# Kernel optimization log

Hardware: AMD Instinct MI355X
Metric: run time of the kernel (lower is better)

## Reference

```python
import jax, jax.numpy as jnp
import numpy as np
import math

HEAD_DIM = 64
RP_DIM = 256
B, H, N = 4, 8, 4096
EPS = 1e-4  # performer positive-feature epsilon


def _ortho_gaussian_matrix(m, d, seed=0):
    # gaussian_orthogonal_random_matrix, scaling=0: stack QR-orthogonalized
    # d x d gaussian blocks, scale rows by norms of an iid gaussian matrix.
    rng = np.random.default_rng(seed)
    blocks = []
    for _ in range(int(np.ceil(m / d))):
        g = rng.standard_normal((d, d))
        q, _ = np.linalg.qr(g)
        blocks.append(q.T)
    mat = np.concatenate(blocks, axis=0)[:m]
    multiplier = np.linalg.norm(rng.standard_normal((m, d)), axis=1)
    return (multiplier[:, None] * mat).astype(np.float32)


def _softmax_features(x, proj, is_query):
    # FAVOR+ positive random features: ratio * exp(Wx - ||x||^2/2 - stab) + eps
    ratio = proj.shape[0] ** -0.5
    xp = jnp.einsum('bhnd,md->bhnm', x, proj)
    diag = 0.5 * jnp.sum(x * x, axis=-1, keepdims=True)
    if is_query:
        stab = jnp.max(xp, axis=-1, keepdims=True)
    else:
        stab = jnp.max(xp, axis=(-1, -2), keepdims=True)
    return ratio * (jnp.exp(xp - diag - stab) + EPS)


def setup_inputs() -> dict:
    key = jax.random.key(0)
    kq, kk, kv = jax.random.split(key, 3)
    Q = jax.random.normal(kq, (B, H, N, HEAD_DIM), dtype=jnp.float32)
    K = jax.random.normal(kk, (B, H, N, HEAD_DIM), dtype=jnp.float32)
    V = jax.random.normal(kv, (B, H, N, HEAD_DIM), dtype=jnp.float32)
    mask = jnp.ones((B, N), dtype=jnp.float32)
    projection = jnp.asarray(_ortho_gaussian_matrix(RP_DIM, HEAD_DIM, seed=0))
    return {'Q': Q, 'K': K, 'V': V, 'mask': mask, 'projection': projection}


def reference(Q, K, V, mask, projection):
    scale = HEAD_DIM ** -0.25  # 1/sqrt(sqrt(head_dim))
    m = mask[:, None, :, None]
    q = Q * scale
    k = K * scale * m
    v = V * m
    phi_q = _softmax_features(q, projection, is_query=True)   # [b,h,n,m]
    phi_k = _softmax_features(k, projection, is_query=False)  # [b,h,n,m]
    # non-causal linear attention
    k_sum = jnp.sum(phi_k, axis=2)                                   # [b,h,m]
    D_inv = 1.0 / jnp.einsum('bhnm,bhm->bhn', phi_q, k_sum)          # [b,h,n]
    context = jnp.einsum('bhnm,bhne->bhme', phi_k, v)                # [b,h,m,e]
    out = jnp.einsum('bhme,bhnm,bhn->bhne', context, phi_q, D_inv)   # [b,h,n,e]
    return out
```

## Files before the change

kernel.cpp:

```cpp
#include <hip/hip_runtime.h>
#include <hip/hip_bf16.h>


typedef __attribute__((ext_vector_type(8))) short short8;
typedef __attribute__((ext_vector_type(4))) float floatx4;

constexpr int BB = 4, HH = 8, NN = 4096, DD = 64, MM = 256, BH = 32;
constexpr float SCALE = 0.3535533905932738f;
constexpr float RATIO = 0.0625f;
constexpr float EPSI  = 1e-4f;
constexpr float NEGINF = -3.4e38f;

__device__ inline unsigned pk2(float a, float b) {
  unsigned ua = __float_as_uint(a) + 0x8000u;
  unsigned ub = __float_as_uint(b) + 0x8000u;
  return (ua >> 16) | (ub & 0xffff0000u);
}
__device__ inline float hif(float x) {
  return __uint_as_float((__float_as_uint(x) + 0x8000u) & 0xffff0000u);
}
__device__ inline unsigned short bhi(float x) {
  return (unsigned short)((__float_as_uint(x) + 0x8000u) >> 16);
}

union Frag { short8 s8; unsigned u[4]; };

__device__ inline void atomicMaxF(float* a, float v) {
  unsigned* ai = (unsigned*)a;
  unsigned old = __atomic_load_n(ai, __ATOMIC_RELAXED);
  while (__uint_as_float(old) < v) {
    unsigned assumed = old;
    old = atomicCAS(ai, assumed, __float_as_uint(v));
    if (old == assumed) break;
  }
}

__global__ __launch_bounds__(256) void prep_kernel(
    const float* __restrict__ proj, unsigned short* __restrict__ projH,
    unsigned short* __restrict__ projL, float* __restrict__ stabk) {
  const int i = blockIdx.x * 256 + threadIdx.x;
  float v = proj[i];
  projH[i] = bhi(v);
  projL[i] = bhi(v - hif(v));
  if (i < BH) stabk[i] = NEGINF;
}

__global__ __launch_bounds__(256) void vsum_kernel(
    const float* __restrict__ V, const float* __restrict__ mask,
    float* __restrict__ Vs) {
  const int bh = blockIdx.y, b = bh >> 3, t = threadIdx.x;
  const int e = t & 63, g = t >> 6;
  const int n0 = blockIdx.x * 128;
  float s = 0.f;
  for (int n = n0 + g; n < n0 + 128; n += 4)
    s += V[((size_t)bh * NN + n) * DD + e] * mask[b * NN + n];
  __shared__ float red[256];
  red[t] = s;
  __syncthreads();
  if (t < 64)
    atomicAdd(&Vs[bh * DD + t], (red[t] + red[t + 64]) + (red[t + 128] + red[t + 192]));
}

__global__ __launch_bounds__(256) void kside_kernel(
    const float* __restrict__ K, const float* __restrict__ V,
    const float* __restrict__ mask, const float* __restrict__ proj,
    float* __restrict__ stabk, float* __restrict__ ksE,
    float* __restrict__ ctxE) {
  const int bh = blockIdx.y, b = bh >> 3;
  const int t = threadIdx.x;
  const int w = t >> 6, l = t & 63, c = l & 15, sq = l >> 4;
  const int m0 = w * 64;

  __shared__ __align__(16) unsigned short sKs[2][32 * 72];
  __shared__ __align__(16) unsigned short sVt[2][64 * 40];
  __shared__ float sDiag[32];
  __shared__ float sRed[4];
  __shared__ __align__(16) unsigned short sPhi[4][4][2][512];

  Frag Bp[4][2][2];
#pragma unroll
  for (int tt = 0; tt < 4; ++tt)
#pragma unroll
    for (int s = 0; s < 2; ++s) {
      const float* pp = proj + (m0 + tt * 16 + c) * DD + s * 32 + sq * 8;
      float4 x0 = *(const float4*)pp;
      float4 x1 = *(const float4*)(pp + 4);
      float v[8] = {x0.x, x0.y, x0.z, x0.w, x1.x, x1.y, x1.z, x1.w};
#pragma unroll
      for (int j = 0; j < 4; ++j) {
        Bp[tt][s][0].u[j] = pk2(v[2 * j], v[2 * j + 1]);
        float l0 = v[2 * j] - hif(v[2 * j]);
        float l1 = v[2 * j + 1] - hif(v[2 * j + 1]);
        Bp[tt][s][1].u[j] = pk2(l0, l1);
      }
    }

  floatx4 ctxacc[4][4];
#pragma unroll
  for (int i = 0; i < 4; ++i)
#pragma unroll
    for (int j = 0; j < 4; ++j) ctxacc[i][j] = (floatx4){0.f, 0.f, 0.f, 0.f};
  float ksac[4] = {0.f, 0.f, 0.f, 0.f};
  float mxloc = NEGINF;

  const int r0 = blockIdx.x * 256;

  for (int ch = 0; ch < 8; ++ch) {
    const int rb = r0 + ch * 32;
    __syncthreads();

#pragma unroll
    for (int rep = 0; rep < 2; ++rep) {
      const int f = t + rep * 256;
      const int n = f >> 4, dg = f & 15;
      const float mk = mask[b * NN + rb + n];
      const float msc = mk * SCALE;
      float4 kv = *(const float4*)(K + ((size_t)bh * NN + rb + n) * DD + dg * 4);
      float k0 = kv.x * msc, k1 = kv.y * msc, k2 = kv.z * msc, k3 = kv.w * msc;
      float ss = fmaf(k0, k0, fmaf(k1, k1, fmaf(k2, k2, k3 * k3)));
      ss += __shfl_xor(ss, 1); ss += __shfl_xor(ss, 2);
      ss += __shfl_xor(ss, 4); ss += __shfl_xor(ss, 8);
      if (dg == 0) sDiag[n] = 0.5f * ss;
      unsigned h0 = pk2(k0, k1), h1 = pk2(k2, k3);
      float q0 = k0 - hif(k0), q1 = k1 - hif(k1);
      float q2 = k2 - hif(k2), q3 = k3 - hif(k3);
      unsigned lo0 = pk2(q0, q1), lo1 = pk2(q2, q3);
      *(uint2*)(&sKs[0][n * 72 + dg * 4]) = make_uint2(h0, h1);
      *(uint2*)(&sKs[1][n * 72 + dg * 4]) = make_uint2(lo0, lo1);
    }
#pragma unroll
    for (int rep = 0; rep < 2; ++rep) {
      const int f = t + rep * 256;
      const int n = f >> 4, eg = f & 15;
      const float mk = mask[b * NN + rb + n];
      float4 vv = *(const float4*)(V + ((size_t)bh * NN + rb + n) * DD + eg * 4);
      float va[4] = {vv.x * mk, vv.y * mk, vv.z * mk, vv.w * mk};
#pragma unroll
      for (int j = 0; j < 4; ++j) {
        sVt[0][(eg * 4 + j) * 40 + n] = bhi(va[j]);
        sVt[1][(eg * 4 + j) * 40 + n] = bhi(va[j] - hif(va[j]));
      }
    }
    __syncthreads();

    Frag Ak[2][2][2];
#pragma unroll
    for (int i = 0; i < 2; ++i)
#pragma unroll
      for (int s = 0; s < 2; ++s) {
        Ak[i][s][0].s8 = *(const short8*)&sKs[0][(i * 16 + c) * 72 + s * 32 + sq * 8];
        Ak[i][s][1].s8 = *(const short8*)&sKs[1][(i * 16 + c) * 72 + s * 32 + sq * 8];
      }
    floatx4 xacc[2][4];
#pragma unroll
    for (int i = 0; i < 2; ++i)
#pragma unroll
      for (int tt = 0; tt < 4; ++tt) {
        floatx4 a = (floatx4){0.f, 0.f, 0.f, 0.f};
#pragma unroll
        for (int s = 0; s < 2; ++s) {
          a = __builtin_amdgcn_mfma_f32_16x16x32_bf16(Ak[i][s][0].s8, Bp[tt][s][0].s8, a, 0, 0, 0);
          a = __builtin_amdgcn_mfma_f32_16x16x32_bf16(Ak[i][s][0].s8, Bp[tt][s][1].s8, a, 0, 0, 0);
          a = __builtin_amdgcn_mfma_f32_16x16x32_bf16(Ak[i][s][1].s8, Bp[tt][s][0].s8, a, 0, 0, 0);
        }
        xacc[i][tt] = a;
      }

    float dg8[2][4];
#pragma unroll
    for (int i = 0; i < 2; ++i)
#pragma unroll
      for (int jj = 0; jj < 4; ++jj) dg8[i][jj] = sDiag[i * 16 + sq * 4 + jj];

    const int qp_c = (sq >> 1);
    const int half = (sq & 1) * 4;
#pragma unroll
    for (int i = 0; i < 2; ++i)
#pragma unroll
      for (int tt = 0; tt < 4; ++tt) {
        float p[4];
#pragma unroll
        for (int jj = 0; jj < 4; ++jj) {
          float xp = xacc[i][tt][jj];
          mxloc = fmaxf(mxloc, xp);
          p[jj] = __expf(xp - dg8[i][jj]);
          ksac[tt] += p[jj];
        }
        unsigned h0 = pk2(p[0], p[1]), h1 = pk2(p[2], p[3]);
        float q0 = p[0] - hif(p[0]), q1 = p[1] - hif(p[1]);
        float q2 = p[2] - hif(p[2]), q3 = p[3] - hif(p[3]);
        unsigned lo0 = pk2(q0, q1), lo1 = pk2(q2, q3);
        const int tl = (i * 2 + qp_c) * 16 + c;
        *(uint2*)(&sPhi[w][tt][0][tl * 8 + half]) = make_uint2(h0, h1);
        *(uint2*)(&sPhi[w][tt][1][tl * 8 + half]) = make_uint2(lo0, lo1);
      }

    Frag Bv[4][2];
#pragma unroll
    for (int E = 0; E < 4; ++E) {
      Bv[E][0].s8 = *(const short8*)&sVt[0][(E * 16 + c) * 40 + sq * 8];
      Bv[E][1].s8 = *(const short8*)&sVt[1][(E * 16 + c) * 40 + sq * 8];
    }
#pragma unroll
    for (int tt = 0; tt < 4; ++tt) {
      Frag Ap[2];
      Ap[0].s8 = *(const short8*)&sPhi[w][tt][0][l * 8];
      Ap[1].s8 = *(const short8*)&sPhi[w][tt][1][l * 8];
#pragma unroll
      for (int E = 0; E < 4; ++E) {
        ctxacc[tt][E] = __builtin_amdgcn_mfma_f32_16x16x32_bf16(Ap[0].s8, Bv[E][0].s8, ctxacc[tt][E], 0, 0, 0);
        ctxacc[tt][E] = __builtin_amdgcn_mfma_f32_16x16x32_bf16(Ap[0].s8, Bv[E][1].s8, ctxacc[tt][E], 0, 0, 0);
        ctxacc[tt][E] = __builtin_amdgcn_mfma_f32_16x16x32_bf16(Ap[1].s8, Bv[E][0].s8, ctxacc[tt][E], 0, 0, 0);
      }
    }
  }

#pragma unroll
  for (int tt = 0; tt < 4; ++tt) {
    float v = ksac[tt];
    v += __shfl_xor(v, 16);
    v += __shfl_xor(v, 32);
    if (sq == 0) atomicAdd(&ksE[bh * MM + m0 + tt * 16 + c], v);
  }
#pragma unroll
  for (int off = 1; off <= 32; off <<= 1) mxloc = fmaxf(mxloc, __shfl_xor(mxloc, off));
  if (l == 0) sRed[w] = mxloc;
  __syncthreads();
  if (t == 0)
    atomicMaxF(&stabk[bh], fmaxf(fmaxf(sRed[0], sRed[1]), fmaxf(sRed[2], sRed[3])));

  float* cg = ctxE + (size_t)bh * MM * DD;
#pragma unroll
  for (int tt = 0; tt < 4; ++tt)
#pragma unroll
    for (int E = 0; E < 4; ++E) {
#pragma unroll
      for (int r = 0; r < 4; ++r) {
        const int m = m0 + tt * 16 + sq * 4 + r;
        const int e = E * 16 + c;
        atomicAdd(&cg[m * DD + e], ctxacc[tt][E][r]);
      }
    }
}

__global__ __launch_bounds__(256) void fixup_kernel(
    const float* __restrict__ stabk, const float* __restrict__ Vs,
    const float* __restrict__ ksE, const float* __restrict__ ctxE,
    float* __restrict__ ksum, float* __restrict__ kssum,
    float* __restrict__ ctxsum, unsigned short* __restrict__ ctxTH,
    unsigned short* __restrict__ ctxTL) {
  const int bh = blockIdx.x, t = threadIdx.x;
  const float es = __expf(-stabk[bh]);
  __shared__ float red[256];

  const float kv = RATIO * (es * ksE[bh * MM + t] + (float)NN * EPSI);
  ksum[bh * MM + t] = kv;
  red[t] = kv;
  __syncthreads();
  for (int off = 128; off >= 1; off >>= 1) {
    if (t < off) red[t] += red[t + off];
    __syncthreads();
  }
  if (t == 0) kssum[bh] = red[0];
  __syncthreads();

  const int e = t & 63, g = t >> 6;
  const float vse = EPSI * Vs[bh * DD + e];
  float cs = 0.f;
  for (int m = g; m < MM; m += 4) {
    float v = RATIO * (es * ctxE[((size_t)bh * MM + m) * DD + e] + vse);
    cs += v;
    ctxTH[((size_t)bh * DD + e) * MM + m] = bhi(v);
    ctxTL[((size_t)bh * DD + e) * MM + m] = bhi(v - hif(v));
  }
  red[t] = cs;
  __syncthreads();
  if (t < 64)
    ctxsum[bh * DD + t] = (red[t] + red[t + 64]) + (red[t + 128] + red[t + 192]);
}

__global__ __launch_bounds__(256, 2) void out_kernel(
    const float* __restrict__ Q,
    const unsigned short* __restrict__ projH, const unsigned short* __restrict__ projL,
    const float* __restrict__ ksum,
    const unsigned short* __restrict__ ctxTH, const unsigned short* __restrict__ ctxTL,
    const float* __restrict__ kssum, const float* __restrict__ ctxsum,
    float* __restrict__ out) {
  const int bh = blockIdx.y;
  const int r0 = blockIdx.x * 64;
  const int t = threadIdx.x, w = t >> 6, l = t & 63, c = l & 15, sq = l >> 4;

  __shared__ __align__(16) unsigned short sQ[2][64 * 80];
  __shared__ __align__(16) unsigned short sP[2][64 * 80];
  __shared__ __align__(16) unsigned short sC[2][64 * 80];
  __shared__ float sKs[256];
  __shared__ float sDiag[64];
  __shared__ __align__(16) unsigned short sPhi[4][2][2][512];

  {
    const int row = t >> 2, q4 = t & 3;
    const float* qp = Q + ((size_t)bh * NN + r0 + row) * DD + q4 * 16;
    float4 t0 = *(const float4*)(qp + 0), t1 = *(const float4*)(qp + 4),
           t2 = *(const float4*)(qp + 8), t3 = *(const float4*)(qp + 12);
    float v[16] = {t0.x, t0.y, t0.z, t0.w, t1.x, t1.y, t1.z, t1.w,
                   t2.x, t2.y, t2.z, t2.w, t3.x, t3.y, t3.z, t3.w};
    float ss = 0.f;
#pragma unroll
    for (int j = 0; j < 16; ++j) { v[j] *= SCALE; ss = fmaf(v[j], v[j], ss); }
    ss += __shfl_xor(ss, 1);
    ss += __shfl_xor(ss, 2);
    if (q4 == 0) sDiag[row] = 0.5f * ss;
    unsigned short* dh = &sQ[0][row * 80 + q4 * 16];
    unsigned short* dl = &sQ[1][row * 80 + q4 * 16];
#pragma unroll
    for (int j = 0; j < 8; ++j) {
      *(unsigned*)&dh[2 * j] = pk2(v[2 * j], v[2 * j + 1]);
      float l0 = v[2 * j] - hif(v[2 * j]), l1 = v[2 * j + 1] - hif(v[2 * j + 1]);
      *(unsigned*)&dl[2 * j] = pk2(l0, l1);
    }
  }
  sKs[t] = ksum[bh * MM + t];
  __syncthreads();

  Frag Bq[2][2];
#pragma unroll
  for (int s = 0; s < 2; ++s)
#pragma unroll
    for (int p = 0; p < 2; ++p)
      Bq[s][p].s8 = *(const short8*)&sQ[p][(w * 16 + c) * 80 + s * 32 + sq * 8];

  const float diagc = sDiag[w * 16 + c];
  floatx4 oacc[4];
#pragma unroll
  for (int E = 0; E < 4; ++E) oacc[E] = (floatx4){0.f, 0.f, 0.f, 0.f};
  float mxacc = NEGINF, dsacc = 0.f;

  for (int mc = 0; mc < 4; ++mc) {
    __syncthreads();
    {
      const int row = t >> 2, q4 = t & 3;
      const size_t gp = (size_t)(mc * 64 + row) * DD + q4 * 16;
      const uint4* ph = (const uint4*)&projH[gp];
      const uint4* pl = (const uint4*)&projL[gp];
      *(uint4*)&sP[0][row * 80 + q4 * 16] = ph[0];
      *(uint4*)&sP[0][row * 80 + q4 * 16 + 8] = ph[1];
      *(uint4*)&sP[1][row * 80 + q4 * 16] = pl[0];
      *(uint4*)&sP[1][row * 80 + q4 * 16 + 8] = pl[1];
      const size_t gc = ((size_t)bh * DD + row) * MM + mc * 64 + q4 * 16;
      const uint4* ch = (const uint4*)&ctxTH[gc];
      const uint4* cl = (const uint4*)&ctxTL[gc];
      *(uint4*)&sC[0][row * 80 + q4 * 16] = ch[0];
      *(uint4*)&sC[0][row * 80 + q4 * 16 + 8] = ch[1];
      *(uint4*)&sC[1][row * 80 + q4 * 16] = cl[0];
      *(uint4*)&sC[1][row * 80 + q4 * 16 + 8] = cl[1];
    }
    __syncthreads();

#pragma unroll
    for (int tt = 0; tt < 4; ++tt) {
      Frag Af[2][2];
#pragma unroll
      for (int s = 0; s < 2; ++s)
#pragma unroll
        for (int p = 0; p < 2; ++p)
          Af[s][p].s8 = *(const short8*)&sP[p][(tt * 16 + c) * 80 + s * 32 + sq * 8];
      floatx4 x = (floatx4){0.f, 0.f, 0.f, 0.f};
#pragma unroll
      for (int s = 0; s < 2; ++s) {
        x = __builtin_amdgcn_mfma_f32_16x16x32_bf16(Af[s][0].s8, Bq[s][0].s8, x, 0, 0, 0);
        x = __builtin_amdgcn_mfma_f32_16x16x32_bf16(Af[s][0].s8, Bq[s][1].s8, x, 0, 0, 0);
        x = __builtin_amdgcn_mfma_f32_16x16x32_bf16(Af[s][1].s8, Bq[s][0].s8, x, 0, 0, 0);
      }
      float p4[4];
#pragma unroll
      for (int jj = 0; jj < 4; ++jj) {
        const float xp = x[jj];
        mxacc = fmaxf(mxacc, xp);
        p4[jj] = __expf(xp - diagc);
        dsacc = fmaf(p4[jj], sKs[mc * 64 + tt * 16 + sq * 4 + jj], dsacc);
      }
      const int kstep = tt >> 1;
      const int tl = ((tt & 1) * 2 + (sq >> 1)) * 16 + c;
      const int off = (sq & 1) * 4;
      float l0 = p4[0] - hif(p4[0]), l1 = p4[1] - hif(p4[1]);
      float l2 = p4[2] - hif(p4[2]), l3 = p4[3] - hif(p4[3]);
      *(uint2*)&sPhi[w][0][kstep][tl * 8 + off] = make_uint2(pk2(p4[0], p4[1]), pk2(p4[2], p4[3]));
      *(uint2*)&sPhi[w][1][kstep][tl * 8 + off] = make_uint2(pk2(l0, l1), pk2(l2, l3));
    }

#pragma unroll
    for (int ks = 0; ks < 2; ++ks) {
      Frag Aph[2];
      Aph[0].s8 = *(const short8*)&sPhi[w][0][ks][l * 8];
      Aph[1].s8 = *(const short8*)&sPhi[w][1][ks][l * 8];
#pragma unroll
      for (int E = 0; E < 4; ++E) {
        Frag Bc0, Bc1;
        Bc0.s8 = *(const short8*)&sC[0][(E * 16 + c) * 80 + ks * 32 + sq * 8];
        Bc1.s8 = *(const short8*)&sC[1][(E * 16 + c) * 80 + ks * 32 + sq * 8];
        oacc[E] = __builtin_amdgcn_mfma_f32_16x16x32_bf16(Aph[0].s8, Bc0.s8, oacc[E], 0, 0, 0);
        oacc[E] = __builtin_amdgcn_mfma_f32_16x16x32_bf16(Aph[0].s8, Bc1.s8, oacc[E], 0, 0, 0);
        oacc[E] = __builtin_amdgcn_mfma_f32_16x16x32_bf16(Aph[1].s8, Bc0.s8, oacc[E], 0, 0, 0);
      }
    }
  }

  mxacc = fmaxf(mxacc, __shfl_xor(mxacc, 16));
  mxacc = fmaxf(mxacc, __shfl_xor(mxacc, 32));
  dsacc += __shfl_xor(dsacc, 16);
  dsacc += __shfl_xor(dsacc, 32);

  const float kss = kssum[bh];
  float fac[4], oinv[4];
#pragma unroll
  for (int jj = 0; jj < 4; ++jj) {
    const int src = sq * 4 + jj;
    const float s_row = __shfl(mxacc, src);
    const float d_row = __shfl(dsacc, src);
    const float f = __expf(s_row) * EPSI;
    fac[jj] = f;
    oinv[jj] = 1.f / (d_row + f * kss);
  }

  const float* csb = ctxsum + bh * DD;
#pragma unroll
  for (int E = 0; E < 4; ++E) {
    const float cse = csb[E * 16 + c];
#pragma unroll
    for (int jj = 0; jj < 4; ++jj) {
      const int row = r0 + w * 16 + sq * 4 + jj;
      out[((size_t)bh * NN + row) * DD + E * 16 + c] =
          (oacc[E][jj] + fac[jj] * cse) * oinv[jj];
    }
  }
}

extern "C" void kernel_launch(void* const* d_in, const int* in_sizes, int n_in,
                              void* d_out, int out_size, void* d_ws, size_t ws_size,
                              hipStream_t stream) {
  const float* Q    = (const float*)d_in[0];
  const float* K    = (const float*)d_in[1];
  const float* V    = (const float*)d_in[2];
  const float* mask = (const float*)d_in[3];
  const float* proj = (const float*)d_in[4];
  float* out = (float*)d_out;

  float* wsf = (float*)d_ws;
  float* stabk  = wsf;
  float* ksum   = wsf + 32;
  float* kssum  = wsf + 8224;
  float* ctxsum = wsf + 8256;
  unsigned short* projH = (unsigned short*)(wsf + 10304);
  unsigned short* projL = (unsigned short*)(wsf + 18496);
  unsigned short* ctxTH = (unsigned short*)(wsf + 26688);
  unsigned short* ctxTL = (unsigned short*)(wsf + 288832);
  float* Vs   = wsf + 550976;
  float* ksE  = wsf + 553024;
  float* ctxE = wsf + 561216;

  hipMemsetAsync(wsf + 550976, 0, (2048 + 8192 + 524288) * sizeof(float), stream);

  prep_kernel<<<64, 256, 0, stream>>>(proj, projH, projL, stabk);
  vsum_kernel<<<dim3(32, BH), 256, 0, stream>>>(V, mask, Vs);
  kside_kernel<<<dim3(16, BH), 256, 0, stream>>>(K, V, mask, proj, stabk, ksE, ctxE);
  fixup_kernel<<<BH, 256, 0, stream>>>(stabk, Vs, ksE, ctxE, ksum, kssum, ctxsum, ctxTH, ctxTL);
  out_kernel<<<dim3(64, BH), 256, 0, stream>>>(Q, projH, projL, ksum, ctxTH, ctxTL, kssum, ctxsum, out);
}
```

Before: 279.8 us.

## Split K-side work finer, reuse bf16 projection, and parallelize ctx fixup transpose

kside_kernel now processes 128 rows per block over twice as many blocks, reads the precomputed bf16 hi/lo projection instead of re-splitting fp32, and interleaves the projection, exp and context MFMAs per tile with a single swizzled phi buffer. The V transpose into LDS now uses lane shuffles so each lane writes packed pairs instead of scattered 16-bit stores. The fixup kernel is split into a k-sum finalizer and a 4x-wider context fixup that transposes through a padded LDS tile for coalesced stores, accumulating ctxsum atomically. The aim is more parallelism and less LDS and global traffic, at the cost of one extra launch and more atomics into ctxE.

```diff
diff --git a/kernel.cpp b/kernel.cpp
--- a/kernel.cpp
+++ b/kernel.cpp
@@ -22,6 +22,7 @@
 __device__ inline unsigned short bhi(float x) {
   return (unsigned short)((__float_as_uint(x) + 0x8000u) >> 16);
 }
+__device__ inline int ph16(int i) { return (i & 56) | ((i + (i >> 3)) & 7); }
 
 union Frag { short8 s8; unsigned u[4]; };
 
@@ -63,7 +64,8 @@
 
 __global__ __launch_bounds__(256) void kside_kernel(
     const float* __restrict__ K, const float* __restrict__ V,
-    const float* __restrict__ mask, const float* __restrict__ proj,
+    const float* __restrict__ mask,
+    const unsigned short* __restrict__ projH, const unsigned short* __restrict__ projL,
     float* __restrict__ stabk, float* __restrict__ ksE,
     float* __restrict__ ctxE) {
   const int bh = blockIdx.y, b = bh >> 3;
@@ -71,28 +73,20 @@
   const int w = t >> 6, l = t & 63, c = l & 15, sq = l >> 4;
   const int m0 = w * 64;
 
-  __shared__ __align__(16) unsigned short sKs[2][32 * 72];
+  __shared__ __align__(16) unsigned short sK[2][32 * 72];
   __shared__ __align__(16) unsigned short sVt[2][64 * 40];
   __shared__ float sDiag[32];
   __shared__ float sRed[4];
-  __shared__ __align__(16) unsigned short sPhi[4][4][2][512];
+  __shared__ __align__(16) unsigned short sPhi[4][2][512];
 
   Frag Bp[4][2][2];
 #pragma unroll
   for (int tt = 0; tt < 4; ++tt)
 #pragma unroll
     for (int s = 0; s < 2; ++s) {
-      const float* pp = proj + (m0 + tt * 16 + c) * DD + s * 32 + sq * 8;
-      float4 x0 = *(const float4*)pp;
-      float4 x1 = *(const float4*)(pp + 4);
-      float v[8] = {x0.x, x0.y, x0.z, x0.w, x1.x, x1.y, x1.z, x1.w};
-#pragma unroll
-      for (int j = 0; j < 4; ++j) {
-        Bp[tt][s][0].u[j] = pk2(v[2 * j], v[2 * j + 1]);
-        float l0 = v[2 * j] - hif(v[2 * j]);
-        float l1 = v[2 * j + 1] - hif(v[2 * j + 1]);
-        Bp[tt][s][1].u[j] = pk2(l0, l1);
-      }
+      const size_t o = (size_t)(m0 + tt * 16 + c) * DD + s * 32 + sq * 8;
+      Bp[tt][s][0].s8 = *(const short8*)&projH[o];
+      Bp[tt][s][1].s8 = *(const short8*)&projL[o];
     }
 
   floatx4 ctxacc[4][4];
@@ -103,9 +97,9 @@
   float ksac[4] = {0.f, 0.f, 0.f, 0.f};
   float mxloc = NEGINF;
 
-  const int r0 = blockIdx.x * 256;
-
-  for (int ch = 0; ch < 8; ++ch) {
+  const int r0 = blockIdx.x * 128;
+
+  for (int ch = 0; ch < 4; ++ch) {
     const int rb = r0 + ch * 32;
     __syncthreads();
 
@@ -124,22 +118,30 @@
       unsigned h0 = pk2(k0, k1), h1 = pk2(k2, k3);
       float q0 = k0 - hif(k0), q1 = k1 - hif(k1);
       float q2 = k2 - hif(k2), q3 = k3 - hif(k3);
-      unsigned lo0 = pk2(q0, q1), lo1 = pk2(q2, q3);
-      *(uint2*)(&sKs[0][n * 72 + dg * 4]) = make_uint2(h0, h1);
-      *(uint2*)(&sKs[1][n * 72 + dg * 4]) = make_uint2(lo0, lo1);
-    }
+      *(uint2*)(&sK[0][n * 72 + dg * 4]) = make_uint2(h0, h1);
+      *(uint2*)(&sK[1][n * 72 + dg * 4]) = make_uint2(pk2(q0, q1), pk2(q2, q3));
+    }
+
 #pragma unroll
     for (int rep = 0; rep < 2; ++rep) {
-      const int f = t + rep * 256;
-      const int n = f >> 4, eg = f & 15;
-      const float mk = mask[b * NN + rb + n];
-      float4 vv = *(const float4*)(V + ((size_t)bh * NN + rb + n) * DD + eg * 4);
+      const int nb = w * 4 + rep * 16;
+      const int n_loc = nb + sq;
+      const float mk = mask[b * NN + rb + n_loc];
+      float4 vv = *(const float4*)(V + ((size_t)bh * NN + rb + n_loc) * DD + c * 4);
       float va[4] = {vv.x * mk, vv.y * mk, vv.z * mk, vv.w * mk};
-#pragma unroll
-      for (int j = 0; j < 4; ++j) {
-        sVt[0][(eg * 4 + j) * 40 + n] = bhi(va[j]);
-        sVt[1][(eg * 4 + j) * 40 + n] = bhi(va[j] - hif(va[j]));
-      }
+      float g[4];
+#pragma unroll
+      for (int k = 0; k < 4; ++k) {
+        const int gi = (sq + k) & 3;
+        float sel = va[(sq - k) & 3];
+        g[gi] = __shfl(sel, gi * 16 + c);
+      }
+      const int estar = c * 4 + sq;
+      unsigned h0 = pk2(g[0], g[1]), h1 = pk2(g[2], g[3]);
+      float q0 = g[0] - hif(g[0]), q1 = g[1] - hif(g[1]);
+      float q2 = g[2] - hif(g[2]), q3 = g[3] - hif(g[3]);
+      *(uint2*)(&sVt[0][estar * 40 + nb]) = make_uint2(h0, h1);
+      *(uint2*)(&sVt[1][estar * 40 + nb]) = make_uint2(pk2(q0, q1), pk2(q2, q3));
     }
     __syncthreads();
 
@@ -148,14 +150,21 @@
     for (int i = 0; i < 2; ++i)
 #pragma unroll
       for (int s = 0; s < 2; ++s) {
-        Ak[i][s][0].s8 = *(const short8*)&sKs[0][(i * 16 + c) * 72 + s * 32 + sq * 8];
-        Ak[i][s][1].s8 = *(const short8*)&sKs[1][(i * 16 + c) * 72 + s * 32 + sq * 8];
-      }
-    floatx4 xacc[2][4];
-#pragma unroll
-    for (int i = 0; i < 2; ++i)
-#pragma unroll
-      for (int tt = 0; tt < 4; ++tt) {
+        Ak[i][s][0].s8 = *(const short8*)&sK[0][(i * 16 + c) * 72 + s * 32 + sq * 8];
+        Ak[i][s][1].s8 = *(const short8*)&sK[1][(i * 16 + c) * 72 + s * 32 + sq * 8];
+      }
+    Frag Bv[4][2];
+#pragma unroll
+    for (int E = 0; E < 4; ++E) {
+      Bv[E][0].s8 = *(const short8*)&sVt[0][(E * 16 + c) * 40 + sq * 8];
+      Bv[E][1].s8 = *(const short8*)&sVt[1][(E * 16 + c) * 40 + sq * 8];
+    }
+
+#pragma unroll
+    for (int tt = 0; tt < 4; ++tt) {
+      floatx4 xacc[2];
+#pragma unroll
+      for (int i = 0; i < 2; ++i) {
         floatx4 a = (floatx4){0.f, 0.f, 0.f, 0.f};
 #pragma unroll
         for (int s = 0; s < 2; ++s) {
@@ -163,49 +172,30 @@
           a = __builtin_amdgcn_mfma_f32_16x16x32_bf16(Ak[i][s][0].s8, Bp[tt][s][1].s8, a, 0, 0, 0);
           a = __builtin_amdgcn_mfma_f32_16x16x32_bf16(Ak[i][s][1].s8, Bp[tt][s][0].s8, a, 0, 0, 0);
         }
-        xacc[i][tt] = a;
-      }
-
-    float dg8[2][4];
-#pragma unroll
-    for (int i = 0; i < 2; ++i)
-#pragma unroll
-      for (int jj = 0; jj < 4; ++jj) dg8[i][jj] = sDiag[i * 16 + sq * 4 + jj];
-
-    const int qp_c = (sq >> 1);
-    const int half = (sq & 1) * 4;
-#pragma unroll
-    for (int i = 0; i < 2; ++i)
-#pragma unroll
-      for (int tt = 0; tt < 4; ++tt) {
+        xacc[i] = a;
+      }
+      const int qp_c = sq >> 1, half = (sq & 1) * 4;
+#pragma unroll
+      for (int i = 0; i < 2; ++i) {
         float p[4];
 #pragma unroll
         for (int jj = 0; jj < 4; ++jj) {
-          float xp = xacc[i][tt][jj];
+          float xp = xacc[i][jj];
           mxloc = fmaxf(mxloc, xp);
-          p[jj] = __expf(xp - dg8[i][jj]);
+          p[jj] = __expf(xp - sDiag[i * 16 + sq * 4 + jj]);
           ksac[tt] += p[jj];
         }
         unsigned h0 = pk2(p[0], p[1]), h1 = pk2(p[2], p[3]);
         float q0 = p[0] - hif(p[0]), q1 = p[1] - hif(p[1]);
         float q2 = p[2] - hif(p[2]), q3 = p[3] - hif(p[3]);
-        unsigned lo0 = pk2(q0, q1), lo1 = pk2(q2, q3);
         const int tl = (i * 2 + qp_c) * 16 + c;
-        *(uint2*)(&sPhi[w][tt][0][tl * 8 + half]) = make_uint2(h0, h1);
-        *(uint2*)(&sPhi[w][tt][1][tl * 8 + half]) = make_uint2(lo0, lo1);
-      }
-
-    Frag Bv[4][2];
-#pragma unroll
-    for (int E = 0; E < 4; ++E) {
-      Bv[E][0].s8 = *(const short8*)&sVt[0][(E * 16 + c) * 40 + sq * 8];
-      Bv[E][1].s8 = *(const short8*)&sVt[1][(E * 16 + c) * 40 + sq * 8];
-    }
-#pragma unroll
-    for (int tt = 0; tt < 4; ++tt) {
+        const int idx = ph16(tl) * 8 + half;
+        *(uint2*)&sPhi[w][0][idx] = make_uint2(h0, h1);
+        *(uint2*)&sPhi[w][1][idx] = make_uint2(pk2(q0, q1), pk2(q2, q3));
+      }
       Frag Ap[2];
-      Ap[0].s8 = *(const short8*)&sPhi[w][tt][0][l * 8];
-      Ap[1].s8 = *(const short8*)&sPhi[w][tt][1][l * 8];
+      Ap[0].s8 = *(const short8*)&sPhi[w][0][ph16(l) * 8];
+      Ap[1].s8 = *(const short8*)&sPhi[w][1][ph16(l) * 8];
 #pragma unroll
       for (int E = 0; E < 4; ++E) {
         ctxacc[tt][E] = __builtin_amdgcn_mfma_f32_16x16x32_bf16(Ap[0].s8, Bv[E][0].s8, ctxacc[tt][E], 0, 0, 0);
@@ -243,16 +233,12 @@
     }
 }
 
-__global__ __launch_bounds__(256) void fixup_kernel(
-    const float* __restrict__ stabk, const float* __restrict__ Vs,
-    const float* __restrict__ ksE, const float* __restrict__ ctxE,
-    float* __restrict__ ksum, float* __restrict__ kssum,
-    float* __restrict__ ctxsum, unsigned short* __restrict__ ctxTH,
-    unsigned short* __restrict__ ctxTL) {
+__global__ __launch_bounds__(256) void ksfin_kernel(
+    const float* __restrict__ stabk, const float* __restrict__ ksE,
+    float* __restrict__ ksum, float* __restrict__ kssum) {
   const int bh = blockIdx.x, t = threadIdx.x;
   const float es = __expf(-stabk[bh]);
   __shared__ float red[256];
-
   const float kv = RATIO * (es * ksE[bh * MM + t] + (float)NN * EPSI);
   ksum[bh * MM + t] = kv;
   red[t] = kv;
@@ -262,21 +248,42 @@
     __syncthreads();
   }
   if (t == 0) kssum[bh] = red[0];
-  __syncthreads();
-
+}
+
+__global__ __launch_bounds__(256) void fixup_kernel(
+    const float* __restrict__ stabk, const float* __restrict__ Vs,
+    const float* __restrict__ ctxE, float* __restrict__ ctxsum,
+    unsigned short* __restrict__ ctxTH, unsigned short* __restrict__ ctxTL) {
+  const int bh = blockIdx.y, mc = blockIdx.x, t = threadIdx.x;
+  const float es = __expf(-stabk[bh]);
   const int e = t & 63, g = t >> 6;
   const float vse = EPSI * Vs[bh * DD + e];
-  float cs = 0.f;
-  for (int m = g; m < MM; m += 4) {
-    float v = RATIO * (es * ctxE[((size_t)bh * MM + m) * DD + e] + vse);
-    cs += v;
-    ctxTH[((size_t)bh * DD + e) * MM + m] = bhi(v);
-    ctxTL[((size_t)bh * DD + e) * MM + m] = bhi(v - hif(v));
-  }
-  red[t] = cs;
+
+  __shared__ float tile[64 * 65];
+  __shared__ float cred[256];
+
+  float csum = 0.f;
+#pragma unroll
+  for (int r = 0; r < 16; ++r) {
+    const int ml = r * 4 + g;
+    float x = ctxE[(size_t)(bh * MM + mc * 64 + ml) * DD + e];
+    float v = RATIO * (es * x + vse);
+    csum += v;
+    tile[e * 65 + ml] = v;
+  }
+  cred[t] = csum;
   __syncthreads();
   if (t < 64)
-    ctxsum[bh * DD + t] = (red[t] + red[t + 64]) + (red[t + 128] + red[t + 192]);
+    atomicAdd(&ctxsum[bh * DD + t],
+              (cred[t] + cred[t + 64]) + (cred[t + 128] + cred[t + 192]));
+#pragma unroll
+  for (int r = 0; r < 16; ++r) {
+    const int el = r * 4 + g, ml = t & 63;
+    float v = tile[el * 65 + ml];
+    const size_t o = ((size_t)(bh * DD + el)) * MM + mc * 64 + ml;
+    ctxTH[o] = bhi(v);
+    ctxTL[o] = bhi(v - hif(v));
+  }
 }
 
 __global__ __launch_bounds__(256, 2) void out_kernel(
@@ -347,12 +354,12 @@
       *(uint4*)&sP[1][row * 80 + q4 * 16] = pl[0];
       *(uint4*)&sP[1][row * 80 + q4 * 16 + 8] = pl[1];
       const size_t gc = ((size_t)bh * DD + row) * MM + mc * 64 + q4 * 16;
-      const uint4* ch = (const uint4*)&ctxTH[gc];
-      const uint4* cl = (const uint4*)&ctxTL[gc];
-      *(uint4*)&sC[0][row * 80 + q4 * 16] = ch[0];
-      *(uint4*)&sC[0][row * 80 + q4 * 16 + 8] = ch[1];
-      *(uint4*)&sC[1][row * 80 + q4 * 16] = cl[0];
-      *(uint4*)&sC[1][row * 80 + q4 * 16 + 8] = cl[1];
+      const uint4* chh = (const uint4*)&ctxTH[gc];
+      const uint4* cll = (const uint4*)&ctxTL[gc];
+      *(uint4*)&sC[0][row * 80 + q4 * 16] = chh[0];
+      *(uint4*)&sC[0][row * 80 + q4 * 16 + 8] = chh[1];
+      *(uint4*)&sC[1][row * 80 + q4 * 16] = cll[0];
+      *(uint4*)&sC[1][row * 80 + q4 * 16 + 8] = cll[1];
     }
     __syncthreads();
 
@@ -449,20 +456,21 @@
   float* stabk  = wsf;
   float* ksum   = wsf + 32;
   float* kssum  = wsf + 8224;
-  float* ctxsum = wsf + 8256;
-  unsigned short* projH = (unsigned short*)(wsf + 10304);
-  unsigned short* projL = (unsigned short*)(wsf + 18496);
-  unsigned short* ctxTH = (unsigned short*)(wsf + 26688);
-  unsigned short* ctxTL = (unsigned short*)(wsf + 288832);
-  float* Vs   = wsf + 550976;
-  float* ksE  = wsf + 553024;
-  float* ctxE = wsf + 561216;
-
-  hipMemsetAsync(wsf + 550976, 0, (2048 + 8192 + 524288) * sizeof(float), stream);
+  unsigned short* projH = (unsigned short*)(wsf + 8256);
+  unsigned short* projL = (unsigned short*)(wsf + 16448);
+  unsigned short* ctxTH = (unsigned short*)(wsf + 24640);
+  unsigned short* ctxTL = (unsigned short*)(wsf + 286784);
+  float* Vs     = wsf + 548928;
+  float* ctxsum = wsf + 550976;
+  float* ksE    = wsf + 553024;
+  float* ctxE   = wsf + 561216;
+
+  hipMemsetAsync(wsf + 548928, 0, (2048 + 2048 + 8192 + 524288) * sizeof(float), stream);
 
   prep_kernel<<<64, 256, 0, stream>>>(proj, projH, projL, stabk);
   vsum_kernel<<<dim3(32, BH), 256, 0, stream>>>(V, mask, Vs);
-  kside_kernel<<<dim3(16, BH), 256, 0, stream>>>(K, V, mask, proj, stabk, ksE, ctxE);
-  fixup_kernel<<<BH, 256, 0, stream>>>(stabk, Vs, ksE, ctxE, ksum, kssum, ctxsum, ctxTH, ctxTL);
+  kside_kernel<<<dim3(32, BH), 256, 0, stream>>>(K, V, mask, projH, projL, stabk, ksE, ctxE);
+  ksfin_kernel<<<BH, 256, 0, stream>>>(stabk, ksE, ksum, kssum);
+  fixup_kernel<<<dim3(4, BH), 256, 0, stream>>>(stabk, Vs, ctxE, ctxsum, ctxTH, ctxTL);
   out_kernel<<<dim3(64, BH), 256, 0, stream>>>(Q, projH, projL, ksum, ctxTH, ctxTL, kssum, ctxsum, out);
 }
```

Result: slower. 299.6 us (+7.1%).
